# Performance work log

Measured on AMD Instinct MI355X. Metric: run time of the kernel, lower is better.

## Reference

```python
import jax, jax.numpy as jnp
import numpy as np

N_NODES = 100000
N_EDGES = 1600000


def _cheb_norm(edge_index, num_nodes):
    # PyG ChebConv norm with sym normalization, lambda_max=2:
    # remove self-loops, L = I - D^-1/2 A D^-1/2, scale by 2/lambda_max (=1),
    # add self-loops with -1 -> diagonal nets to 0, leaving w = -d^-1/2 d^-1/2 on edges.
    src, dst = edge_index[0], edge_index[1]
    mask = (src != dst).astype(jnp.float32)  # remove_self_loops
    deg = jax.ops.segment_sum(mask, src, num_segments=num_nodes)
    dinv = jnp.where(deg > 0, jax.lax.rsqrt(jnp.maximum(deg, 1.0)), 0.0)
    w = -dinv[src] * dinv[dst] * mask
    return w


def _cheb_conv(x, src, dst, w_edge, W, b, num_nodes):
    # W: [K=3, C_in, C_out], Chebyshev recurrence T0=x, T1=Lx, T2=2L T1 - T0
    def prop(h):
        return jax.ops.segment_sum(w_edge[:, None] * h[src], dst, num_segments=num_nodes)

    tx0 = x
    tx1 = prop(x)
    tx2 = 2.0 * prop(tx1) - tx0
    out = tx0 @ W[0] + tx1 @ W[1] + tx2 @ W[2] + b
    return out


def setup_inputs() -> dict:
    key = jax.random.key(0)
    ks = jax.random.split(key, 10)
    x = jax.random.normal(ks[0], (N_NODES, 128), dtype=jnp.float32)
    edge_index = jax.random.randint(ks[1], (2, N_EDGES), 0, N_NODES, dtype=jnp.int64)
    batch = jnp.zeros((N_NODES,), dtype=jnp.int64)

    def glorot(k, shape):
        fan = shape[-2] + shape[-1]
        return jax.random.uniform(k, shape, jnp.float32, -1.0, 1.0) * np.sqrt(6.0 / fan)

    W1 = glorot(ks[2], (3, 128, 64))
    b1 = jnp.zeros((64,), jnp.float32)
    W2 = glorot(ks[3], (3, 64, 128))
    b2 = jnp.zeros((128,), jnp.float32)
    W3 = glorot(ks[4], (3, 128, 256))
    b3 = jnp.zeros((256,), jnp.float32)
    return {"x": x, "edge_index": edge_index, "batch": batch,
            "W1": W1, "b1": b1, "W2": W2, "b2": b2, "W3": W3, "b3": b3}


def reference(x, edge_index, batch, W1, b1, W2, b2, W3, b3):
    num_nodes = x.shape[0]
    src, dst = edge_index[0], edge_index[1]
    w_edge = _cheb_norm(edge_index, num_nodes)
    h = jax.nn.relu(_cheb_conv(x, src, dst, w_edge, W1, b1, num_nodes))
    h = jax.nn.relu(_cheb_conv(h, src, dst, w_edge, W2, b2, num_nodes))
    h = _cheb_conv(h, src, dst, w_edge, W3, b3, num_nodes)
    return h
```

## Files before the change

### kernel.cpp

```cpp
#include <hip/hip_runtime.h>

#define N_NODES 100000
#define N_EDGES 1600000
#define CAP 64

typedef short short8 __attribute__((ext_vector_type(8)));
typedef float f32x4 __attribute__((ext_vector_type(4)));

__device__ __forceinline__ unsigned short f2b(float f) {
    unsigned u = __builtin_bit_cast(unsigned, f);
    u += 0x7fffu + ((u >> 16) & 1u);
    return (unsigned short)(u >> 16);
}
__device__ __forceinline__ float b2f_lo(unsigned p) {
    return __builtin_bit_cast(float, p << 16);
}
__device__ __forceinline__ float b2f_hi(unsigned p) {
    return __builtin_bit_cast(float, p & 0xffff0000u);
}
__device__ __forceinline__ float b2f(unsigned short s) {
    return __builtin_bit_cast(float, ((unsigned)s) << 16);
}

__global__ void k_f2b(const float* __restrict__ in, unsigned short* __restrict__ out, int n4) {
    int i = blockIdx.x * blockDim.x + threadIdx.x;
    if (i < n4) {
        float4 v = ((const float4*)in)[i];
        uint2 o;
        o.x = (unsigned)f2b(v.x) | ((unsigned)f2b(v.y) << 16);
        o.y = (unsigned)f2b(v.z) | ((unsigned)f2b(v.w) << 16);
        ((uint2*)out)[i] = o;
    }
}

__global__ void k_wt(const float* __restrict__ W, unsigned short* __restrict__ Wt,
                     int KT, int COUT) {
    int i = blockIdx.x * blockDim.x + threadIdx.x;
    if (i < KT * COUT) {
        int k = i % KT, n = i / KT;
        Wt[(size_t)n * KT + k] = f2b(W[(size_t)k * COUT + n]);
    }
}

__global__ void k_build(const int* __restrict__ src, const int* __restrict__ dst,
                        float* __restrict__ degout, int* __restrict__ cnt,
                        int* __restrict__ slots) {
    int e = blockIdx.x * blockDim.x + threadIdx.x;
    if (e < N_EDGES) {
        int s = src[e], d = dst[e];
        if (s != d) {
            atomicAdd(&degout[s], 1.0f);
            int pos = atomicAdd(&cnt[d], 1);
            if (pos < CAP) slots[(size_t)d * CAP + pos] = s;
        }
    }
}

__global__ void k_dinv(float* __restrict__ deg) {
    int n = blockIdx.x * blockDim.x + threadIdx.x;
    if (n < N_NODES) {
        float dg = deg[n];
        deg[n] = dg > 0.f ? rsqrtf(dg) : 0.f;
    }
}

template <int C>
__global__ __launch_bounds__(256) void k_gather3(const unsigned short* __restrict__ h,
                                                 const int* __restrict__ cnt,
                                                 const int* __restrict__ slots,
                                                 const float* __restrict__ dinv,
                                                 float alpha, const unsigned short* __restrict__ init,
                                                 float beta, unsigned short* __restrict__ out) {
    const int wave = threadIdx.x >> 6;
    const int lane = threadIdx.x & 63;
    const int n = blockIdx.x * 4 + wave;
    if (n >= N_NODES) return;
    const int m = min(cnt[n], CAP);
    const float scale = -alpha * dinv[n];

    int col = 0;
    float w = 0.f;
    if (lane < m) {
        col = slots[(size_t)n * CAP + lane];
        w = dinv[col];
    }
    const int wi = __builtin_bit_cast(int, w);

    if (C == 128) {
        const unsigned* h2 = (const unsigned*)h;
        float ax = 0.f, ay = 0.f;
        int j = 0;
        for (; j + 4 <= m; j += 4) {
            int c0 = __builtin_amdgcn_readlane(col, j + 0);
            int c1 = __builtin_amdgcn_readlane(col, j + 1);
            int c2 = __builtin_amdgcn_readlane(col, j + 2);
            int c3 = __builtin_amdgcn_readlane(col, j + 3);
            float w0 = __builtin_bit_cast(float, __builtin_amdgcn_readlane(wi, j + 0));
            float w1 = __builtin_bit_cast(float, __builtin_amdgcn_readlane(wi, j + 1));
            float w2 = __builtin_bit_cast(float, __builtin_amdgcn_readlane(wi, j + 2));
            float w3 = __builtin_bit_cast(float, __builtin_amdgcn_readlane(wi, j + 3));
            unsigned q0 = h2[(size_t)c0 * 64 + lane];
            unsigned q1 = h2[(size_t)c1 * 64 + lane];
            unsigned q2 = h2[(size_t)c2 * 64 + lane];
            unsigned q3 = h2[(size_t)c3 * 64 + lane];
            ax = fmaf(w0, b2f_lo(q0), ax); ay = fmaf(w0, b2f_hi(q0), ay);
            ax = fmaf(w1, b2f_lo(q1), ax); ay = fmaf(w1, b2f_hi(q1), ay);
            ax = fmaf(w2, b2f_lo(q2), ax); ay = fmaf(w2, b2f_hi(q2), ay);
            ax = fmaf(w3, b2f_lo(q3), ax); ay = fmaf(w3, b2f_hi(q3), ay);
        }
        for (; j < m; j++) {
            int c0 = __builtin_amdgcn_readlane(col, j);
            float w0 = __builtin_bit_cast(float, __builtin_amdgcn_readlane(wi, j));
            unsigned q0 = h2[(size_t)c0 * 64 + lane];
            ax = fmaf(w0, b2f_lo(q0), ax); ay = fmaf(w0, b2f_hi(q0), ay);
        }
        float vx = scale * ax, vy = scale * ay;
        if (init) {
            unsigned ip = ((const unsigned*)init)[(size_t)n * 64 + lane];
            vx = fmaf(beta, b2f_lo(ip), vx);
            vy = fmaf(beta, b2f_hi(ip), vy);
        }
        ((unsigned*)out)[(size_t)n * 64 + lane] =
            (unsigned)f2b(vx) | ((unsigned)f2b(vy) << 16);
    } else {
        float a = 0.f;
        int j = 0;
        for (; j + 4 <= m; j += 4) {
            int c0 = __builtin_amdgcn_readlane(col, j + 0);
            int c1 = __builtin_amdgcn_readlane(col, j + 1);
            int c2 = __builtin_amdgcn_readlane(col, j + 2);
            int c3 = __builtin_amdgcn_readlane(col, j + 3);
            float w0 = __builtin_bit_cast(float, __builtin_amdgcn_readlane(wi, j + 0));
            float w1 = __builtin_bit_cast(float, __builtin_amdgcn_readlane(wi, j + 1));
            float w2 = __builtin_bit_cast(float, __builtin_amdgcn_readlane(wi, j + 2));
            float w3 = __builtin_bit_cast(float, __builtin_amdgcn_readlane(wi, j + 3));
            float v0 = b2f(h[(size_t)c0 * 64 + lane]);
            float v1 = b2f(h[(size_t)c1 * 64 + lane]);
            float v2 = b2f(h[(size_t)c2 * 64 + lane]);
            float v3 = b2f(h[(size_t)c3 * 64 + lane]);
            a = fmaf(w0, v0, a); a = fmaf(w1, v1, a);
            a = fmaf(w2, v2, a); a = fmaf(w3, v3, a);
        }
        for (; j < m; j++) {
            int c0 = __builtin_amdgcn_readlane(col, j);
            float w0 = __builtin_bit_cast(float, __builtin_amdgcn_readlane(wi, j));
            a = fmaf(w0, b2f(h[(size_t)c0 * 64 + lane]), a);
        }
        float v = scale * a;
        if (init) v = fmaf(beta, b2f(init[(size_t)n * 64 + lane]), v);
        out[(size_t)n * 64 + lane] = f2b(v);
    }
}

template <int CIN, int COUT, int NSL, bool RELU, bool BF16OUT>
__global__ __launch_bounds__(256) void k_mm2(const unsigned short* __restrict__ t0,
                                             const unsigned short* __restrict__ t1,
                                             const unsigned short* __restrict__ t2,
                                             const unsigned short* __restrict__ Wt,
                                             const float* __restrict__ bias,
                                             void* __restrict__ outv) {
    constexpr int KT = 3 * CIN;
    constexpr int KP = KT + 8;
    constexpr int NFR = NSL / 16;
    __shared__ unsigned short sw[NSL * KP];

    const int tid = threadIdx.x;
    const int n0 = blockIdx.y * NSL;

    constexpr int CHUNKS = NSL * KT / 8;
    for (int i = tid; i < CHUNKS; i += 256) {
        int row = i / (KT / 8);
        int k8 = i % (KT / 8);
        short8 v = *(const short8*)(Wt + (size_t)(n0 + row) * KT + k8 * 8);
        *(short8*)(sw + row * KP + k8 * 8) = v;
    }
    __syncthreads();

    const int wave = tid >> 6, lane = tid & 63;
    const int l16 = lane & 15, quad = lane >> 4;
    const int mBase = blockIdx.x * 128 + wave * 32;
    const int r0 = mBase + l16, r1 = mBase + 16 + l16;
    const bool in0 = r0 < N_NODES, in1 = r1 < N_NODES;

    f32x4 acc[2][NFR] = {};
    const unsigned short* tb[3] = {t0, t1, t2};
    const short8 zero8 = {0, 0, 0, 0, 0, 0, 0, 0};

    #pragma unroll
    for (int kt = 0; kt < KT / 32; kt++) {
        const int kb = kt * 32;
        const unsigned short* t = tb[kb / CIN];
        const int kin = (kb % CIN) + quad * 8;
        short8 a0 = zero8, a1 = zero8;
        if (in0) a0 = *(const short8*)(t + (size_t)r0 * CIN + kin);
        if (in1) a1 = *(const short8*)(t + (size_t)r1 * CIN + kin);
        #pragma unroll
        for (int nf = 0; nf < NFR; nf++) {
            const short8 b = *(const short8*)(sw + (nf * 16 + l16) * KP + kb + quad * 8);
            acc[0][nf] = __builtin_amdgcn_mfma_f32_16x16x32_bf16(a0, b, acc[0][nf], 0, 0, 0);
            acc[1][nf] = __builtin_amdgcn_mfma_f32_16x16x32_bf16(a1, b, acc[1][nf], 0, 0, 0);
        }
    }

    #pragma unroll
    for (int mi = 0; mi < 2; mi++) {
        #pragma unroll
        for (int nf = 0; nf < NFR; nf++) {
            #pragma unroll
            for (int r = 0; r < 4; r++) {
                const int node = mBase + mi * 16 + quad * 4 + r;
                if (node < N_NODES) {
                    const int co = n0 + nf * 16 + l16;
                    float o = acc[mi][nf][r] + bias[co];
                    if (RELU) o = fmaxf(o, 0.f);
                    if (BF16OUT)
                        ((unsigned short*)outv)[(size_t)node * COUT + co] = f2b(o);
                    else
                        ((float*)outv)[(size_t)node * COUT + co] = o;
                }
            }
        }
    }
}

static inline int ceil_div(int a, int b) { return (a + b - 1) / b; }

extern "C" void kernel_launch(void* const* d_in, const int* in_sizes, int n_in,
                              void* d_out, int out_size, void* d_ws, size_t ws_size,
                              hipStream_t stream) {
    const float* x   = (const float*)d_in[0];
    const int*   ei  = (const int*)d_in[1];
    const int*   src = ei;
    const int*   dst = ei + N_EDGES;
    const float* W1 = (const float*)d_in[3];
    const float* b1 = (const float*)d_in[4];
    const float* W2 = (const float*)d_in[5];
    const float* b2 = (const float*)d_in[6];
    const float* W3 = (const float*)d_in[7];
    const float* b3 = (const float*)d_in[8];
    float* out = (float*)d_out;

    char* p = (char*)d_ws;
    int*   slots  = (int*)p;             p += (size_t)N_NODES * CAP * 4;
    float* dinv   = (float*)p;           p += (size_t)N_NODES * 4;
    int*   cnt    = (int*)p;             p += (size_t)N_NODES * 4;
    unsigned short* xb   = (unsigned short*)p; p += (size_t)N_NODES * 128 * 2;
    unsigned short* tx1b = (unsigned short*)p; p += (size_t)N_NODES * 128 * 2;
    unsigned short* tx2b = (unsigned short*)p; p += (size_t)N_NODES * 128 * 2;
    unsigned short* h1b  = (unsigned short*)p; p += (size_t)N_NODES * 64 * 2;
    unsigned short* h2b  = (unsigned short*)p; p += (size_t)N_NODES * 128 * 2;
    unsigned short* Wt1  = (unsigned short*)p; p += (size_t)64 * 384 * 2;
    unsigned short* Wt2  = (unsigned short*)p; p += (size_t)128 * 192 * 2;
    unsigned short* Wt3  = (unsigned short*)p; p += (size_t)256 * 384 * 2;

    const int TB = 256;
    const int gE = ceil_div(N_EDGES, TB);
    const int gN = ceil_div(N_NODES, TB);
    const int gG = ceil_div(N_NODES, 4);
    const int gM = ceil_div(N_NODES, 128);

    k_f2b<<<ceil_div(N_NODES * 128 / 4, TB), TB, 0, stream>>>(x, xb, N_NODES * 128 / 4);
    k_wt<<<ceil_div(384 * 64, TB), TB, 0, stream>>>(W1, Wt1, 384, 64);
    k_wt<<<ceil_div(192 * 128, TB), TB, 0, stream>>>(W2, Wt2, 192, 128);
    k_wt<<<ceil_div(384 * 256, TB), TB, 0, stream>>>(W3, Wt3, 384, 256);

    hipMemsetAsync(dinv, 0, N_NODES * sizeof(float), stream);
    hipMemsetAsync(cnt, 0, N_NODES * sizeof(int), stream);
    k_build<<<gE, TB, 0, stream>>>(src, dst, dinv, cnt, slots);
    k_dinv<<<gN, TB, 0, stream>>>(dinv);

    k_gather3<128><<<gG, TB, 0, stream>>>(xb, cnt, slots, dinv, 1.f, nullptr, 0.f, tx1b);
    k_gather3<128><<<gG, TB, 0, stream>>>(tx1b, cnt, slots, dinv, 2.f, xb, -1.f, tx2b);
    k_mm2<128, 64, 64, true, true><<<dim3(gM, 1), TB, 0, stream>>>(xb, tx1b, tx2b, Wt1, b1, h1b);

    k_gather3<64><<<gG, TB, 0, stream>>>(h1b, cnt, slots, dinv, 1.f, nullptr, 0.f, tx1b);
    k_gather3<64><<<gG, TB, 0, stream>>>(tx1b, cnt, slots, dinv, 2.f, h1b, -1.f, tx2b);
    k_mm2<64, 128, 128, true, true><<<dim3(gM, 1), TB, 0, stream>>>(h1b, tx1b, tx2b, Wt2, b2, h2b);

    k_gather3<128><<<gG, TB, 0, stream>>>(h2b, cnt, slots, dinv, 1.f, nullptr, 0.f, tx1b);
    k_gather3<128><<<gG, TB, 0, stream>>>(tx1b, cnt, slots, dinv, 2.f, h2b, -1.f, tx2b);
    k_mm2<128, 256, 64, false, false><<<dim3(gM, 4), TB, 0, stream>>>(h2b, tx1b, tx2b, Wt3, b3, out);
}
```

Before: 843.8 us.

## Gather two nodes per wavefront with half-wave vectorized neighbor loads

```diff
diff --git a/kernel.cpp b/kernel.cpp
--- a/kernel.cpp
+++ b/kernel.cpp
@@ -65,7 +65,7 @@
 }
 
 template <int C>
-__global__ __launch_bounds__(256) void k_gather3(const unsigned short* __restrict__ h,
+__global__ __launch_bounds__(256) void k_gather4(const unsigned short* __restrict__ h,
                                                  const int* __restrict__ cnt,
                                                  const int* __restrict__ slots,
                                                  const float* __restrict__ dinv,
@@ -73,82 +73,100 @@
                                                  float beta, unsigned short* __restrict__ out) {
     const int wave = threadIdx.x >> 6;
     const int lane = threadIdx.x & 63;
-    const int n = blockIdx.x * 4 + wave;
-    if (n >= N_NODES) return;
-    const int m = min(cnt[n], CAP);
-    const float scale = -alpha * dinv[n];
-
-    int col = 0;
-    float w = 0.f;
-    if (lane < m) {
-        col = slots[(size_t)n * CAP + lane];
-        w = dinv[col];
-    }
-    const int wi = __builtin_bit_cast(int, w);
+    const int half = lane >> 5;
+    const int l32  = lane & 31;
+    const int n0 = (blockIdx.x * 4 + wave) * 2;
+    if (n0 >= N_NODES) return;
+    const int n1 = n0 + 1;
+    const int m0 = min(cnt[n0], CAP);
+    const int m1 = min(cnt[n1], CAP);
+    const int nMy = half ? n1 : n0;
+    const int mMy = half ? m1 : m0;
+    (void)mMy;
+
+    int c0l = 0, c1l = 0;
+    float w0f = 0.f, w1f = 0.f;
+    if (lane < m0) { c0l = slots[(size_t)n0 * CAP + lane]; w0f = dinv[c0l]; }
+    if (lane < m1) { c1l = slots[(size_t)n1 * CAP + lane]; w1f = dinv[c1l]; }
+    const int w0i = __builtin_bit_cast(int, w0f);
+    const int w1i = __builtin_bit_cast(int, w1f);
+
+    const int mlo = min(m0, m1), mhi = max(m0, m1);
+    const float scale = -alpha * dinv[nMy];
 
     if (C == 128) {
+        const uint2* h4 = (const uint2*)h;
+        float ax = 0.f, ay = 0.f, az = 0.f, aw = 0.f;
+        int j = 0;
+        for (; j + 4 <= mlo; j += 4) {
+            #pragma unroll
+            for (int k = 0; k < 4; k++) {
+                int cA = __builtin_amdgcn_readlane(c0l, j + k);
+                int cB = __builtin_amdgcn_readlane(c1l, j + k);
+                float wA = __builtin_bit_cast(float, __builtin_amdgcn_readlane(w0i, j + k));
+                float wB = __builtin_bit_cast(float, __builtin_amdgcn_readlane(w1i, j + k));
+                int c = half ? cB : cA;
+                float w = half ? wB : wA;
+                uint2 q = h4[(size_t)c * 32 + l32];
+                ax = fmaf(w, b2f_lo(q.x), ax); ay = fmaf(w, b2f_hi(q.x), ay);
+                az = fmaf(w, b2f_lo(q.y), az); aw = fmaf(w, b2f_hi(q.y), aw);
+            }
+        }
+        for (; j < mhi; j++) {
+            int cA = __builtin_amdgcn_readlane(c0l, j);
+            int cB = __builtin_amdgcn_readlane(c1l, j);
+            float wA = __builtin_bit_cast(float, __builtin_amdgcn_readlane(w0i, j));
+            float wB = __builtin_bit_cast(float, __builtin_amdgcn_readlane(w1i, j));
+            int c = half ? cB : cA;
+            float w = half ? wB : wA;
+            uint2 q = h4[(size_t)c * 32 + l32];
+            ax = fmaf(w, b2f_lo(q.x), ax); ay = fmaf(w, b2f_hi(q.x), ay);
+            az = fmaf(w, b2f_lo(q.y), az); aw = fmaf(w, b2f_hi(q.y), aw);
+        }
+        float vx = scale * ax, vy = scale * ay, vz = scale * az, vw = scale * aw;
+        if (init) {
+            uint2 ip = ((const uint2*)init)[(size_t)nMy * 32 + l32];
+            vx = fmaf(beta, b2f_lo(ip.x), vx); vy = fmaf(beta, b2f_hi(ip.x), vy);
+            vz = fmaf(beta, b2f_lo(ip.y), vz); vw = fmaf(beta, b2f_hi(ip.y), vw);
+        }
+        uint2 o;
+        o.x = (unsigned)f2b(vx) | ((unsigned)f2b(vy) << 16);
+        o.y = (unsigned)f2b(vz) | ((unsigned)f2b(vw) << 16);
+        ((uint2*)out)[(size_t)nMy * 32 + l32] = o;
+    } else {
         const unsigned* h2 = (const unsigned*)h;
         float ax = 0.f, ay = 0.f;
         int j = 0;
-        for (; j + 4 <= m; j += 4) {
-            int c0 = __builtin_amdgcn_readlane(col, j + 0);
-            int c1 = __builtin_amdgcn_readlane(col, j + 1);
-            int c2 = __builtin_amdgcn_readlane(col, j + 2);
-            int c3 = __builtin_amdgcn_readlane(col, j + 3);
-            float w0 = __builtin_bit_cast(float, __builtin_amdgcn_readlane(wi, j + 0));
-            float w1 = __builtin_bit_cast(float, __builtin_amdgcn_readlane(wi, j + 1));
-            float w2 = __builtin_bit_cast(float, __builtin_amdgcn_readlane(wi, j + 2));
-            float w3 = __builtin_bit_cast(float, __builtin_amdgcn_readlane(wi, j + 3));
-            unsigned q0 = h2[(size_t)c0 * 64 + lane];
-            unsigned q1 = h2[(size_t)c1 * 64 + lane];
-            unsigned q2 = h2[(size_t)c2 * 64 + lane];
-            unsigned q3 = h2[(size_t)c3 * 64 + lane];
-            ax = fmaf(w0, b2f_lo(q0), ax); ay = fmaf(w0, b2f_hi(q0), ay);
-            ax = fmaf(w1, b2f_lo(q1), ax); ay = fmaf(w1, b2f_hi(q1), ay);
-            ax = fmaf(w2, b2f_lo(q2), ax); ay = fmaf(w2, b2f_hi(q2), ay);
-            ax = fmaf(w3, b2f_lo(q3), ax); ay = fmaf(w3, b2f_hi(q3), ay);
-        }
-        for (; j < m; j++) {
-            int c0 = __builtin_amdgcn_readlane(col, j);
-            float w0 = __builtin_bit_cast(float, __builtin_amdgcn_readlane(wi, j));
-            unsigned q0 = h2[(size_t)c0 * 64 + lane];
-            ax = fmaf(w0, b2f_lo(q0), ax); ay = fmaf(w0, b2f_hi(q0), ay);
+        for (; j + 4 <= mlo; j += 4) {
+            #pragma unroll
+            for (int k = 0; k < 4; k++) {
+                int cA = __builtin_amdgcn_readlane(c0l, j + k);
+                int cB = __builtin_amdgcn_readlane(c1l, j + k);
+                float wA = __builtin_bit_cast(float, __builtin_amdgcn_readlane(w0i, j + k));
+                float wB = __builtin_bit_cast(float, __builtin_amdgcn_readlane(w1i, j + k));
+                int c = half ? cB : cA;
+                float w = half ? wB : wA;
+                unsigned q = h2[(size_t)c * 32 + l32];
+                ax = fmaf(w, b2f_lo(q), ax); ay = fmaf(w, b2f_hi(q), ay);
+            }
+        }
+        for (; j < mhi; j++) {
+            int cA = __builtin_amdgcn_readlane(c0l, j);
+            int cB = __builtin_amdgcn_readlane(c1l, j);
+            float wA = __builtin_bit_cast(float, __builtin_amdgcn_readlane(w0i, j));
+            float wB = __builtin_bit_cast(float, __builtin_amdgcn_readlane(w1i, j));
+            int c = half ? cB : cA;
+            float w = half ? wB : wA;
+            unsigned q = h2[(size_t)c * 32 + l32];
+            ax = fmaf(w, b2f_lo(q), ax); ay = fmaf(w, b2f_hi(q), ay);
         }
         float vx = scale * ax, vy = scale * ay;
         if (init) {
-            unsigned ip = ((const unsigned*)init)[(size_t)n * 64 + lane];
-            vx = fmaf(beta, b2f_lo(ip), vx);
-            vy = fmaf(beta, b2f_hi(ip), vy);
-        }
-        ((unsigned*)out)[(size_t)n * 64 + lane] =
+            unsigned ip = ((const unsigned*)init)[(size_t)nMy * 32 + l32];
+            vx = fmaf(beta, b2f_lo(ip), vx); vy = fmaf(beta, b2f_hi(ip), vy);
+        }
+        ((unsigned*)out)[(size_t)nMy * 32 + l32] =
             (unsigned)f2b(vx) | ((unsigned)f2b(vy) << 16);
-    } else {
-        float a = 0.f;
-        int j = 0;
-        for (; j + 4 <= m; j += 4) {
-            int c0 = __builtin_amdgcn_readlane(col, j + 0);
-            int c1 = __builtin_amdgcn_readlane(col, j + 1);
-            int c2 = __builtin_amdgcn_readlane(col, j + 2);
-            int c3 = __builtin_amdgcn_readlane(col, j + 3);
-            float w0 = __builtin_bit_cast(float, __builtin_amdgcn_readlane(wi, j + 0));
-            float w1 = __builtin_bit_cast(float, __builtin_amdgcn_readlane(wi, j + 1));
-            float w2 = __builtin_bit_cast(float, __builtin_amdgcn_readlane(wi, j + 2));
-            float w3 = __builtin_bit_cast(float, __builtin_amdgcn_readlane(wi, j + 3));
-            float v0 = b2f(h[(size_t)c0 * 64 + lane]);
-            float v1 = b2f(h[(size_t)c1 * 64 + lane]);
-            float v2 = b2f(h[(size_t)c2 * 64 + lane]);
-            float v3 = b2f(h[(size_t)c3 * 64 + lane]);
-            a = fmaf(w0, v0, a); a = fmaf(w1, v1, a);
-            a = fmaf(w2, v2, a); a = fmaf(w3, v3, a);
-        }
-        for (; j < m; j++) {
-            int c0 = __builtin_amdgcn_readlane(col, j);
-            float w0 = __builtin_bit_cast(float, __builtin_amdgcn_readlane(wi, j));
-            a = fmaf(w0, b2f(h[(size_t)c0 * 64 + lane]), a);
-        }
-        float v = scale * a;
-        if (init) v = fmaf(beta, b2f(init[(size_t)n * 64 + lane]), v);
-        out[(size_t)n * 64 + lane] = f2b(v);
     }
 }
 
@@ -256,7 +274,7 @@
     const int TB = 256;
     const int gE = ceil_div(N_EDGES, TB);
     const int gN = ceil_div(N_NODES, TB);
-    const int gG = ceil_div(N_NODES, 4);
+    const int gG = ceil_div(N_NODES, 8);
     const int gM = ceil_div(N_NODES, 128);
 
     k_f2b<<<ceil_div(N_NODES * 128 / 4, TB), TB, 0, stream>>>(x, xb, N_NODES * 128 / 4);
@@ -269,15 +287,15 @@
     k_build<<<gE, TB, 0, stream>>>(src, dst, dinv, cnt, slots);
     k_dinv<<<gN, TB, 0, stream>>>(dinv);
 
-    k_gather3<128><<<gG, TB, 0, stream>>>(xb, cnt, slots, dinv, 1.f, nullptr, 0.f, tx1b);
-    k_gather3<128><<<gG, TB, 0, stream>>>(tx1b, cnt, slots, dinv, 2.f, xb, -1.f, tx2b);
+    k_gather4<128><<<gG, TB, 0, stream>>>(xb, cnt, slots, dinv, 1.f, nullptr, 0.f, tx1b);
+    k_gather4<128><<<gG, TB, 0, stream>>>(tx1b, cnt, slots, dinv, 2.f, xb, -1.f, tx2b);
     k_mm2<128, 64, 64, true, true><<<dim3(gM, 1), TB, 0, stream>>>(xb, tx1b, tx2b, Wt1, b1, h1b);
 
-    k_gather3<64><<<gG, TB, 0, stream>>>(h1b, cnt, slots, dinv, 1.f, nullptr, 0.f, tx1b);
-    k_gather3<64><<<gG, TB, 0, stream>>>(tx1b, cnt, slots, dinv, 2.f, h1b, -1.f, tx2b);
+    k_gather4<64><<<gG, TB, 0, stream>>>(h1b, cnt, slots, dinv, 1.f, nullptr, 0.f, tx1b);
+    k_gather4<64><<<gG, TB, 0, stream>>>(tx1b, cnt, slots, dinv, 2.f, h1b, -1.f, tx2b);
     k_mm2<64, 128, 128, true, true><<<dim3(gM, 1), TB, 0, stream>>>(h1b, tx1b, tx2b, Wt2, b2, h2b);
 
-    k_gather3<128><<<gG, TB, 0, stream>>>(h2b, cnt, slots, dinv, 1.f, nullptr, 0.f, tx1b);
-    k_gather3<128><<<gG, TB, 0, stream>>>(tx1b, cnt, slots, dinv, 2.f, h2b, -1.f, tx2b);
+    k_gather4<128><<<gG, TB, 0, stream>>>(h2b, cnt, slots, dinv, 1.f, nullptr, 0.f, tx1b);
+    k_gather4<128><<<gG, TB, 0, stream>>>(tx1b, cnt, slots, dinv, 2.f, h2b, -1.f, tx2b);
     k_mm2<128, 256, 64, false, false><<<dim3(gM, 4), TB, 0, stream>>>(h2b, tx1b, tx2b, Wt3, b3, out);
 }
```

New measurement: 848.3 us. No clear change (+0.5%).
